# Kernel tuning notes

Measured on AMD Instinct MI355X. Metric: run time of the kernel, lower is better.

The kernel has to match this reference:

```python
import jax, jax.numpy as jnp
import numpy as np

B, T, C, E = 8, 2048, 2048, 16
DE = C // E          # per-expert width = 128
H = 4 * DE           # expert hidden = 512


def setup_inputs() -> dict:
    key = jax.random.key(0)
    ks = jax.random.split(key, 7)
    s = 0.02
    return {
        "x": jax.random.normal(ks[0], (B, T, C), dtype=jnp.float32),
        "gate_w": jax.random.normal(ks[1], (E, C), dtype=jnp.float32) * s,
        "gate_b": jnp.zeros((E,), dtype=jnp.float32),
        "fc_w": jax.random.normal(ks[2], (E, H, DE), dtype=jnp.float32) * s,
        "fc_b": jnp.zeros((E, H), dtype=jnp.float32),
        "proj_w": jax.random.normal(ks[3], (E, DE, H), dtype=jnp.float32) * s,
        "proj_b": jnp.zeros((E, DE), dtype=jnp.float32),
    }


def _thres_hot(logits):
    # ThresHot: hard threshold at 0 with straight-through gradient.
    hard = (logits > 0).astype(logits.dtype)
    return logits + jax.lax.stop_gradient(hard - logits)


def reference(x, gate_w, gate_b, fc_w, fc_b, proj_w, proj_b):
    b, t, c = x.shape
    e = gate_b.shape[0]
    de = c // e
    # gate: [b,t,E]
    logits = jnp.einsum("btc,ec->bte", x, gate_w) + gate_b
    gw = _thres_hot(logits)
    # chunk channels: expert index is the FASTEST-varying dim (torch view(b,t,de,E))
    xc = x.reshape(b, t, de, e)  # [b,t,de,E]
    # per-expert MLP: fc -> gelu(exact) -> proj  (dropout=0)
    h = jnp.einsum("btde,ehd->bteh", xc, fc_w) + fc_b          # [b,t,E,H]
    h = jax.nn.gelu(h, approximate=False)
    out = jnp.einsum("bteh,edh->bted", h, proj_w) + proj_b      # [b,t,E,de]
    # weighted combine; torch stacks experts at dim=2 then flattens (de fastest)
    return (gw[..., None] * out).reshape(b, t, c)
```

## Files before the change

kernel.cpp:

```cpp
#include <hip/hip_runtime.h>

#define N_TOK 16384
#define C_DIM 2048
#define E_NUM 16
#define DE_DIM 128
#define H_DIM 512

typedef __attribute__((ext_vector_type(8))) short bf16x8;
typedef __attribute__((ext_vector_type(4))) float f32x4;

__device__ __forceinline__ unsigned short f2bf(float f) {
    unsigned int u = __float_as_uint(f);
    unsigned int r = u + 0x7fffu + ((u >> 16) & 1u);
    return (unsigned short)(r >> 16);
}

__device__ __forceinline__ uint4 pack8(float4 a, float4 b) {
    return make_uint4(
        (unsigned int)f2bf(a.x) | ((unsigned int)f2bf(a.y) << 16),
        (unsigned int)f2bf(a.z) | ((unsigned int)f2bf(a.w) << 16),
        (unsigned int)f2bf(b.x) | ((unsigned int)f2bf(b.y) << 16),
        (unsigned int)f2bf(b.z) | ((unsigned int)f2bf(b.w) << 16));
}

__device__ __forceinline__ float gelu_erf(float v) {
    float z  = v * 0.70710678118654752f;
    float az = fabsf(z);
    float t  = __builtin_amdgcn_rcpf(1.0f + 0.3275911f * az);
    float poly = t * (0.254829592f + t * (-0.284496736f + t * (1.421413741f +
                 t * (-1.453152027f + t * 1.061405429f))));
    float ex = __expf(-z * z);
    float er = copysignf(1.0f - poly * ex, z);
    return 0.5f * v * (1.0f + er);
}

__global__ __launch_bounds__(256) void moe_conv_w(
    const float* __restrict__ fcw, const float* __restrict__ pjw,
    unsigned short* __restrict__ fcwb, unsigned short* __restrict__ pjwb)
{
    const int id = blockIdx.x * 256 + threadIdx.x;
    {
        const int base = id * 8;
        const int d0 = base & 127;
        const int h  = (base >> 7) & 511;
        const int dd = d0 ^ ((h & 7) << 3);
        float4 a = *reinterpret_cast<const float4*>(fcw + base);
        float4 b = *reinterpret_cast<const float4*>(fcw + base + 4);
        *reinterpret_cast<uint4*>(fcwb + (base & ~127) + dd) = pack8(a, b);
    }
    {
        const int base = id * 8;
        const int h0 = base & 511;
        const int d  = (base >> 9) & 127;
        const int hh = h0 ^ ((d & 7) << 3);
        float4 a = *reinterpret_cast<const float4*>(pjw + base);
        float4 b = *reinterpret_cast<const float4*>(pjw + base + 4);
        *reinterpret_cast<uint4*>(pjwb + (base & ~511) + hh) = pack8(a, b);
    }
}

__global__ __launch_bounds__(256) void moe_gate(
    const float* __restrict__ xg,
    const float* __restrict__ gw,
    const float* __restrict__ gb,
    float* __restrict__ gwf)
{
    __shared__ float gws[16 * 256];

    const int t  = threadIdx.x;
    const int n0 = blockIdx.x * 32;
    const int nl = t >> 3;
    const int p  = t & 7;

    double dacc[16];
#pragma unroll
    for (int e = 0; e < 16; ++e) dacc[e] = 0.0;

    for (int cc = 0; cc < 8; ++cc) {
        __syncthreads();
#pragma unroll
        for (int ii = 0; ii < 4; ++ii) {
            int fi = ii * 1024 + t * 4;
            int e = fi >> 8, cl = fi & 255;
            *reinterpret_cast<float4*>(&gws[e * 256 + cl]) =
                *reinterpret_cast<const float4*>(gw + (size_t)e * 2048 + cc * 256 + cl);
        }
        __syncthreads();
#pragma unroll
        for (int i = 0; i < 4; ++i) {
            const int cl = p * 8 + i * 64;
            const float* xr = xg + (size_t)(n0 + nl) * 2048 + cc * 256 + cl;
            float4 xa = *reinterpret_cast<const float4*>(xr);
            float4 xb = *reinterpret_cast<const float4*>(xr + 4);
            double xd0 = xa.x, xd1 = xa.y, xd2 = xa.z, xd3 = xa.w;
            double xd4 = xb.x, xd5 = xb.y, xd6 = xb.z, xd7 = xb.w;
#pragma unroll
            for (int e = 0; e < 16; ++e) {
                float4 ga = *reinterpret_cast<const float4*>(&gws[e * 256 + cl]);
                float4 gv = *reinterpret_cast<const float4*>(&gws[e * 256 + cl + 4]);
                double s = dacc[e];
                s = fma(xd0, (double)ga.x, s);
                s = fma(xd1, (double)ga.y, s);
                s = fma(xd2, (double)ga.z, s);
                s = fma(xd3, (double)ga.w, s);
                s = fma(xd4, (double)gv.x, s);
                s = fma(xd5, (double)gv.y, s);
                s = fma(xd6, (double)gv.z, s);
                s = fma(xd7, (double)gv.w, s);
                dacc[e] = s;
            }
        }
    }
#pragma unroll
    for (int e = 0; e < 16; ++e) {
        double v = dacc[e];
        v += __shfl_xor(v, 1);
        v += __shfl_xor(v, 2);
        v += __shfl_xor(v, 4);
        dacc[e] = v;
    }
    const int e0 = 2 * p;
    float g0 = (dacc[e0]     + (double)gb[e0]     > 0.0) ? 1.0f : 0.0f;
    float g1 = (dacc[e0 + 1] + (double)gb[e0 + 1] > 0.0) ? 1.0f : 0.0f;
    float2* gout = reinterpret_cast<float2*>(gwf + (size_t)(n0 + nl) * 16 + e0);
    *gout = make_float2(g0, g1);
}

template<int PRE>
__global__ __launch_bounds__(256, 2) void moe_expert_mlp(
    const float* __restrict__ xg,
    const float* __restrict__ fcw,
    const float* __restrict__ fcb,
    const float* __restrict__ pjw,
    const float* __restrict__ pjb,
    const unsigned short* __restrict__ fcwb,
    const unsigned short* __restrict__ pjwb,
    const float* __restrict__ gwf,
    float* __restrict__ y)
{
    __shared__ unsigned short W1s[64 * 136];
    __shared__ unsigned short W2s[128 * 72];
    __shared__ unsigned short Hs[4 * 32 * 72];

    const int t    = threadIdx.x;
    const int wid  = t >> 6;
    const int lane = t & 63;
    const int q    = lane >> 4;
    const int m    = lane & 15;
    const int raw = blockIdx.x;
    const int e   = (raw >> 3) & 15;
    const int tb  = (raw & 7) | ((raw >> 7) << 3);
    const int n0  = tb * 128 + wid * 32;

    bf16x8 a1[2][4];
#pragma unroll
    for (int tm = 0; tm < 2; ++tm)
#pragma unroll
        for (int kk = 0; kk < 4; ++kk) {
            const float* base = xg + (size_t)(n0 + tm * 16 + m) * 2048
                              + (kk * 32 + q * 8) * 16 + e;
            union { unsigned short u[8]; bf16x8 v; } pk;
#pragma unroll
            for (int j = 0; j < 8; ++j) pk.u[j] = f2bf(base[j * 16]);
            a1[tm][kk] = pk.v;
        }

    f32x4 oacc[2][8];
#pragma unroll
    for (int tm = 0; tm < 2; ++tm)
#pragma unroll
        for (int tn = 0; tn < 8; ++tn) oacc[tm][tn] = (f32x4){0.f, 0.f, 0.f, 0.f};

    unsigned short* HsW = &Hs[wid * 32 * 72];
    const char* W1b = reinterpret_cast<const char*>(W1s);
    const char* W2b = reinterpret_cast<const char*>(W2s);

    for (int hc = 0; hc < 8; ++hc) {
        __syncthreads();
        if constexpr (PRE) {
            const unsigned short* g1 = fcwb + ((size_t)e * 512 + hc * 64) * 128;
            const unsigned short* g2 = pjwb + (size_t)e * 128 * 512 + hc * 64;
#pragma unroll
            for (int it = 0; it < 4; ++it) {
                const int s = it * 2048 + t * 8;
                __builtin_amdgcn_global_load_lds(
                    (const __attribute__((address_space(1))) unsigned int*)(g1 + s),
                    (__attribute__((address_space(3))) unsigned int*)(&W1s[s]), 16, 0, 0);
            }
#pragma unroll
            for (int it = 0; it < 4; ++it) {
                const int s = it * 2048 + t * 8;
                __builtin_amdgcn_global_load_lds(
                    (const __attribute__((address_space(1))) unsigned int*)
                        (g2 + (size_t)(s >> 6) * 512 + (s & 63)),
                    (__attribute__((address_space(3))) unsigned int*)(&W2s[s]), 16, 0, 0);
            }
        } else {
#pragma unroll
            for (int it = 0; it < 4; ++it) {
                int idx = it * 256 + t;
                int hh = idx >> 4, ds = (idx & 15) * 8;
                const float* src = fcw + ((size_t)e * 512 + hc * 64 + hh) * 128 + ds;
                float4 va = *reinterpret_cast<const float4*>(src);
                float4 vb = *reinterpret_cast<const float4*>(src + 4);
                *reinterpret_cast<uint4*>(&W1s[hh * 136 + ds]) = pack8(va, vb);
            }
#pragma unroll
            for (int it = 0; it < 4; ++it) {
                int idx = it * 256 + t;
                int d = idx >> 3, cs = (idx & 7) * 8;
                const float* src = pjw + ((size_t)e * 128 + d) * 512 + hc * 64 + cs;
                float4 va = *reinterpret_cast<const float4*>(src);
                float4 vb = *reinterpret_cast<const float4*>(src + 4);
                *reinterpret_cast<uint4*>(&W2s[d * 72 + cs]) = pack8(va, vb);
            }
        }
        __syncthreads();

        f32x4 h1[2][4];
#pragma unroll
        for (int tm = 0; tm < 2; ++tm)
#pragma unroll
            for (int tn = 0; tn < 4; ++tn) h1[tm][tn] = (f32x4){0.f, 0.f, 0.f, 0.f};
#pragma unroll
        for (int kk = 0; kk < 4; ++kk) {
#pragma unroll
            for (int tn = 0; tn < 4; ++tn) {
                bf16x8 b;
                if constexpr (PRE) {
                    const int r = tn * 16 + m;
                    b = *reinterpret_cast<const bf16x8*>(
                        W1b + r * 256 + (((kk * 32 + q * 8) * 2) ^ ((r & 7) << 4)));
                } else {
                    b = *reinterpret_cast<const bf16x8*>(
                        &W1s[(tn * 16 + m) * 136 + kk * 32 + q * 8]);
                }
                h1[0][tn] = __builtin_amdgcn_mfma_f32_16x16x32_bf16(a1[0][kk], b, h1[0][tn], 0, 0, 0);
                h1[1][tn] = __builtin_amdgcn_mfma_f32_16x16x32_bf16(a1[1][kk], b, h1[1][tn], 0, 0, 0);
            }
        }
#pragma unroll
        for (int tn = 0; tn < 4; ++tn) {
            float bias = fcb[e * 512 + hc * 64 + tn * 16 + m];
#pragma unroll
            for (int tm = 0; tm < 2; ++tm)
#pragma unroll
                for (int r = 0; r < 4; ++r) {
                    float g = gelu_erf(h1[tm][tn][r] + bias);
                    HsW[(tm * 16 + q * 4 + r) * 72 + tn * 16 + m] = f2bf(g);
                }
        }
        __asm__ volatile("" ::: "memory");

#pragma unroll
        for (int kk2 = 0; kk2 < 2; ++kk2) {
            bf16x8 a2_0 = *reinterpret_cast<const bf16x8*>(&HsW[(m) * 72 + kk2 * 32 + q * 8]);
            bf16x8 a2_1 = *reinterpret_cast<const bf16x8*>(&HsW[(16 + m) * 72 + kk2 * 32 + q * 8]);
#pragma unroll
            for (int tn2 = 0; tn2 < 8; ++tn2) {
                bf16x8 b2;
                if constexpr (PRE) {
                    const int r2 = tn2 * 16 + m;
                    b2 = *reinterpret_cast<const bf16x8*>(
                        W2b + r2 * 128 + (((kk2 * 32 + q * 8) * 2) ^ ((r2 & 7) << 4)));
                } else {
                    b2 = *reinterpret_cast<const bf16x8*>(
                        &W2s[(tn2 * 16 + m) * 72 + kk2 * 32 + q * 8]);
                }
                oacc[0][tn2] = __builtin_amdgcn_mfma_f32_16x16x32_bf16(a2_0, b2, oacc[0][tn2], 0, 0, 0);
                oacc[1][tn2] = __builtin_amdgcn_mfma_f32_16x16x32_bf16(a2_1, b2, oacc[1][tn2], 0, 0, 0);
            }
        }
    }

    float gwv[2][4];
#pragma unroll
    for (int tm = 0; tm < 2; ++tm)
#pragma unroll
        for (int r = 0; r < 4; ++r)
            gwv[tm][r] = gwf[(size_t)(n0 + tm * 16 + q * 4 + r) * 16 + e];
#pragma unroll
    for (int tn2 = 0; tn2 < 8; ++tn2) {
        float pb = pjb[e * 128 + tn2 * 16 + m];
#pragma unroll
        for (int tm = 0; tm < 2; ++tm)
#pragma unroll
            for (int r = 0; r < 4; ++r) {
                float v = (oacc[tm][tn2][r] + pb) * gwv[tm][r];
                y[(size_t)(n0 + tm * 16 + q * 4 + r) * 2048 + e * 128 + tn2 * 16 + m] = v;
            }
    }
}

extern "C" void kernel_launch(void* const* d_in, const int* in_sizes, int n_in,
                              void* d_out, int out_size, void* d_ws, size_t ws_size,
                              hipStream_t stream) {
    const float* x      = (const float*)d_in[0];
    const float* gate_w = (const float*)d_in[1];
    const float* gate_b = (const float*)d_in[2];
    const float* fc_w   = (const float*)d_in[3];
    const float* fc_b   = (const float*)d_in[4];
    const float* proj_w = (const float*)d_in[5];
    const float* proj_b = (const float*)d_in[6];
    float* y            = (float*)d_out;

    const size_t gwf_bytes = (size_t)N_TOK * E_NUM * 4;
    const size_t wb_bytes  = (size_t)E_NUM * H_DIM * DE_DIM * 2;
    float* gwf = (float*)d_ws;
    unsigned short* fcwb = (unsigned short*)((char*)d_ws + gwf_bytes);
    unsigned short* pjwb = (unsigned short*)((char*)d_ws + gwf_bytes + wb_bytes);
    const int use_pre = (ws_size >= gwf_bytes + 2 * wb_bytes) ? 1 : 0;

    if (use_pre)
        moe_conv_w<<<dim3(512), dim3(256), 0, stream>>>(fc_w, proj_w, fcwb, pjwb);
    moe_gate<<<dim3(N_TOK / 32), dim3(256), 0, stream>>>(x, gate_w, gate_b, gwf);
    if (use_pre)
        moe_expert_mlp<1><<<dim3(E_NUM * (N_TOK / 128)), dim3(256), 0, stream>>>(
            x, fc_w, fc_b, proj_w, proj_b, fcwb, pjwb, gwf, y);
    else
        moe_expert_mlp<0><<<dim3(E_NUM * (N_TOK / 128)), dim3(256), 0, stream>>>(
            x, fc_w, fc_b, proj_w, proj_b, fcwb, pjwb, gwf, y);
}
```

Measured before the change: 452.3 us.

## Halve tokens per gate block and shrink padded LDS tiles in precomputed path

The gate kernel now handles 16 tokens per block, with 16 threads per token each reading one float4 per 64-column group. That doubles the grid and gives more coalesced x reads, but reloads the gate weights into LDS twice as often. The reduction gains one more shuffle level, and a single thread writes all 16 gate flags. In the expert MLP, the precomputed-weight path sizes W1s/W2s without padding to cut LDS use and possibly raise occupancy.

```diff
diff --git a/kernel.cpp b/kernel.cpp
--- a/kernel.cpp
+++ b/kernel.cpp
@@ -68,9 +68,9 @@
     __shared__ float gws[16 * 256];
 
     const int t  = threadIdx.x;
-    const int n0 = blockIdx.x * 32;
-    const int nl = t >> 3;
-    const int p  = t & 7;
+    const int n0 = blockIdx.x * 16;
+    const int nl = t >> 4;
+    const int p  = t & 15;
 
     double dacc[16];
 #pragma unroll
@@ -87,26 +87,19 @@
         }
         __syncthreads();
 #pragma unroll
-        for (int i = 0; i < 4; ++i) {
-            const int cl = p * 8 + i * 64;
-            const float* xr = xg + (size_t)(n0 + nl) * 2048 + cc * 256 + cl;
-            float4 xa = *reinterpret_cast<const float4*>(xr);
-            float4 xb = *reinterpret_cast<const float4*>(xr + 4);
+        for (int g = 0; g < 4; ++g) {
+            const int cl = g * 64 + p * 4;
+            float4 xa = *reinterpret_cast<const float4*>(
+                xg + (size_t)(n0 + nl) * 2048 + cc * 256 + cl);
             double xd0 = xa.x, xd1 = xa.y, xd2 = xa.z, xd3 = xa.w;
-            double xd4 = xb.x, xd5 = xb.y, xd6 = xb.z, xd7 = xb.w;
 #pragma unroll
             for (int e = 0; e < 16; ++e) {
                 float4 ga = *reinterpret_cast<const float4*>(&gws[e * 256 + cl]);
-                float4 gv = *reinterpret_cast<const float4*>(&gws[e * 256 + cl + 4]);
                 double s = dacc[e];
                 s = fma(xd0, (double)ga.x, s);
                 s = fma(xd1, (double)ga.y, s);
                 s = fma(xd2, (double)ga.z, s);
                 s = fma(xd3, (double)ga.w, s);
-                s = fma(xd4, (double)gv.x, s);
-                s = fma(xd5, (double)gv.y, s);
-                s = fma(xd6, (double)gv.z, s);
-                s = fma(xd7, (double)gv.w, s);
                 dacc[e] = s;
             }
         }
@@ -117,13 +110,20 @@
         v += __shfl_xor(v, 1);
         v += __shfl_xor(v, 2);
         v += __shfl_xor(v, 4);
+        v += __shfl_xor(v, 8);
         dacc[e] = v;
     }
-    const int e0 = 2 * p;
-    float g0 = (dacc[e0]     + (double)gb[e0]     > 0.0) ? 1.0f : 0.0f;
-    float g1 = (dacc[e0 + 1] + (double)gb[e0 + 1] > 0.0) ? 1.0f : 0.0f;
-    float2* gout = reinterpret_cast<float2*>(gwf + (size_t)(n0 + nl) * 16 + e0);
-    *gout = make_float2(g0, g1);
+    if (p == 0) {
+        float g[16];
+#pragma unroll
+        for (int e = 0; e < 16; ++e)
+            g[e] = (dacc[e] + (double)gb[e] > 0.0) ? 1.0f : 0.0f;
+        float4* o = reinterpret_cast<float4*>(gwf + (size_t)(n0 + nl) * 16);
+        o[0] = make_float4(g[0],  g[1],  g[2],  g[3]);
+        o[1] = make_float4(g[4],  g[5],  g[6],  g[7]);
+        o[2] = make_float4(g[8],  g[9],  g[10], g[11]);
+        o[3] = make_float4(g[12], g[13], g[14], g[15]);
+    }
 }
 
 template<int PRE>
@@ -138,8 +138,10 @@
     const float* __restrict__ gwf,
     float* __restrict__ y)
 {
-    __shared__ unsigned short W1s[64 * 136];
-    __shared__ unsigned short W2s[128 * 72];
+    constexpr int W1S = PRE ? 128 : 136;
+    constexpr int W2S = PRE ? 64  : 72;
+    __shared__ unsigned short W1s[64 * W1S];
+    __shared__ unsigned short W2s[128 * W2S];
     __shared__ unsigned short Hs[4 * 32 * 72];
 
     const int t    = threadIdx.x;
@@ -203,7 +205,7 @@
                 const float* src = fcw + ((size_t)e * 512 + hc * 64 + hh) * 128 + ds;
                 float4 va = *reinterpret_cast<const float4*>(src);
                 float4 vb = *reinterpret_cast<const float4*>(src + 4);
-                *reinterpret_cast<uint4*>(&W1s[hh * 136 + ds]) = pack8(va, vb);
+                *reinterpret_cast<uint4*>(&W1s[hh * W1S + ds]) = pack8(va, vb);
             }
 #pragma unroll
             for (int it = 0; it < 4; ++it) {
@@ -212,7 +214,7 @@
                 const float* src = pjw + ((size_t)e * 128 + d) * 512 + hc * 64 + cs;
                 float4 va = *reinterpret_cast<const float4*>(src);
                 float4 vb = *reinterpret_cast<const float4*>(src + 4);
-                *reinterpret_cast<uint4*>(&W2s[d * 72 + cs]) = pack8(va, vb);
+                *reinterpret_cast<uint4*>(&W2s[d * W2S + cs]) = pack8(va, vb);
             }
         }
         __syncthreads();
@@ -233,7 +235,7 @@
                         W1b + r * 256 + (((kk * 32 + q * 8) * 2) ^ ((r & 7) << 4)));
                 } else {
                     b = *reinterpret_cast<const bf16x8*>(
-                        &W1s[(tn * 16 + m) * 136 + kk * 32 + q * 8]);
+                        &W1s[(tn * 16 + m) * W1S + kk * 32 + q * 8]);
                 }
                 h1[0][tn] = __builtin_amdgcn_mfma_f32_16x16x32_bf16(a1[0][kk], b, h1[0][tn], 0, 0, 0);
                 h1[1][tn] = __builtin_amdgcn_mfma_f32_16x16x32_bf16(a1[1][kk], b, h1[1][tn], 0, 0, 0);
@@ -265,7 +267,7 @@
                         W2b + r2 * 128 + (((kk2 * 32 + q * 8) * 2) ^ ((r2 & 7) << 4)));
                 } else {
                     b2 = *reinterpret_cast<const bf16x8*>(
-                        &W2s[(tn2 * 16 + m) * 72 + kk2 * 32 + q * 8]);
+                        &W2s[(tn2 * 16 + m) * W2S + kk2 * 32 + q * 8]);
                 }
                 oacc[0][tn2] = __builtin_amdgcn_mfma_f32_16x16x32_bf16(a2_0, b2, oacc[0][tn2], 0, 0, 0);
                 oacc[1][tn2] = __builtin_amdgcn_mfma_f32_16x16x32_bf16(a2_1, b2, oacc[1][tn2], 0, 0, 0);
@@ -313,7 +315,7 @@
 
     if (use_pre)
         moe_conv_w<<<dim3(512), dim3(256), 0, stream>>>(fc_w, proj_w, fcwb, pjwb);
-    moe_gate<<<dim3(N_TOK / 32), dim3(256), 0, stream>>>(x, gate_w, gate_b, gwf);
+    moe_gate<<<dim3(N_TOK / 16), dim3(256), 0, stream>>>(x, gate_w, gate_b, gwf);
     if (use_pre)
         moe_expert_mlp<1><<<dim3(E_NUM * (N_TOK / 128)), dim3(256), 0, stream>>>(
             x, fc_w, fc_b, proj_w, proj_b, fcwb, pjwb, gwf, y);
```

Result: no change. 452.0 us (-0.1%).
